# Performance work log

Hardware: AMD Instinct MI355X
Metric: run time of the kernel (lower is better)

## Reference

```python
import jax, jax.numpy as jnp
import numpy as np

B, N, E = 8, 20000, 320000
D_IN, D, D_OUT = 1, 64, 1
EPS = 1e-5


def _layer_norm(z, gamma, beta):
    mu = z.mean(-1, keepdims=True)
    var = ((z - mu) ** 2).mean(-1, keepdims=True)
    return gamma * (z - mu) / jnp.sqrt(var + EPS) + beta


def _mp_layer(h, src, dst, Ws, Wm, bias, gamma, beta):
    # h: (B, N, D); src/dst: (E,)
    h_self = h @ Ws                          # (B, N, D)
    msg = h[:, src, :] @ Wm                  # (B, E, D) gather + GEMM
    h_agg = jnp.zeros_like(h).at[:, dst, :].add(msg)   # scatter-add over nodes
    deg = jnp.zeros((N,), h.dtype).at[dst].add(1.0)
    deg = jnp.maximum(deg, 1.0)
    h_agg = h_agg / deg[None, :, None]
    z = h + jax.nn.relu(h_self + h_agg + bias)  # dropout = identity (eval)
    return _layer_norm(z, gamma, beta)


def setup_inputs() -> dict:
    key = jax.random.key(0)
    ks = jax.random.split(key, 16)
    # weights stored (in, out); y = x @ W + b. Kaiming-normal-ish scale.
    def kaiming(k, fin, fout):
        return jax.random.normal(k, (fin, fout), jnp.float32) * np.sqrt(2.0 / fin)
    inp = {
        "x": jax.random.normal(ks[0], (B, N, D_IN), jnp.float32),
        "edge_index": jax.random.randint(ks[1], (2, E), 0, N),
        "W_in": kaiming(ks[2], D_IN, D), "b_in": jnp.zeros((D,), jnp.float32),
        "Ws1": kaiming(ks[3], D, D), "Wm1": kaiming(ks[4], D, D),
        "bias1": jnp.zeros((D,), jnp.float32),
        "g1": jnp.ones((D,), jnp.float32), "be1": jnp.zeros((D,), jnp.float32),
        "Ws2": kaiming(ks[5], D, D), "Wm2": kaiming(ks[6], D, D),
        "bias2": jnp.zeros((D,), jnp.float32),
        "g2": jnp.ones((D,), jnp.float32), "be2": jnp.zeros((D,), jnp.float32),
        "Wh1": kaiming(ks[7], 2 * D, D), "bh1": jnp.zeros((D,), jnp.float32),
        "Wh2": kaiming(ks[8], D, D_OUT), "bh2": jnp.zeros((D_OUT,), jnp.float32),
    }
    return inp


def reference(x, edge_index, W_in, b_in, Ws1, Wm1, bias1, g1, be1,
              Ws2, Wm2, bias2, g2, be2, Wh1, bh1, Wh2, bh2):
    src, dst = edge_index[0], edge_index[1]
    h = jax.nn.relu(x @ W_in + b_in)                       # (B, N, D)
    h = _mp_layer(h, src, dst, Ws1, Wm1, bias1, g1, be1)
    h = _mp_layer(h, src, dst, Ws2, Wm2, bias2, g2, be2)
    graph_emb = jnp.concatenate([h.mean(axis=1), h.max(axis=1)], axis=-1)  # (B, 2D)
    out = jax.nn.relu(graph_emb @ Wh1 + bh1) @ Wh2 + bh2   # (B, D_OUT)
    return out
```

## Files before the change

### kernel.cpp

```cpp
#include <hip/hip_runtime.h>

#define BB 8
#define NN 20000
#define EE 320000
#define DD 64
#define ROWS (BB*NN)
#define TILES (ROWS/16)
#define EPS 1e-5f
#define CH 64


typedef __attribute__((ext_vector_type(4))) float float4v;
typedef __attribute__((ext_vector_type(8))) _Float16 half8v;
typedef __attribute__((ext_vector_type(4))) _Float16 half4v;

__device__ __forceinline__ int bcasti(int v, int l) {
  return __builtin_amdgcn_readlane(v, l);
}

__global__ __launch_bounds__(256) void k_encoder(const float* __restrict__ x,
    const float* __restrict__ Win, const float* __restrict__ bin,
    float* __restrict__ hN, _Float16* __restrict__ hH) {
  int idx = blockIdx.x * 256 + threadIdx.x;
  int g = idx * 4;
  if (g < NN * 512) {
    int n = g >> 9;
    int b = (g >> 6) & 7;
    int d0 = g & 63;
    float xv = x[(size_t)b * NN + n];
    float4 wv = *(const float4*)&Win[d0];
    float4 bv = *(const float4*)&bin[d0];
    float4 o;
    o.x = fmaf(xv, wv.x, bv.x); o.x = o.x > 0.f ? o.x : 0.f;
    o.y = fmaf(xv, wv.y, bv.y); o.y = o.y > 0.f ? o.y : 0.f;
    o.z = fmaf(xv, wv.z, bv.z); o.z = o.z > 0.f ? o.z : 0.f;
    o.w = fmaf(xv, wv.w, bv.w); o.w = o.w > 0.f ? o.w : 0.f;
    *(float4*)&hN[g] = o;
    half4v ho;
    ho[0] = (_Float16)o.x; ho[1] = (_Float16)o.y;
    ho[2] = (_Float16)o.z; ho[3] = (_Float16)o.w;
    *(half4v*)&hH[g] = ho;
  }
}

__global__ __launch_bounds__(256) void k_deg(const int* __restrict__ dst,
                                             int* __restrict__ cnt) {
  int e = blockIdx.x * 256 + threadIdx.x;
  if (e < EE) atomicAdd(&cnt[dst[e]], 1);
}

__global__ __launch_bounds__(1024) void k_scan(const int* __restrict__ cnt,
                                               int* __restrict__ rowptr) {
  __shared__ int part[1024];
  int t = threadIdx.x;
  const int PER = (NN + 1023) / 1024;
  int base = t * PER;
  int s = 0;
#pragma unroll
  for (int i = 0; i < PER; ++i) {
    int idx = base + i;
    s += (idx < NN) ? cnt[idx] : 0;
  }
  part[t] = s;
  __syncthreads();
  for (int off = 1; off < 1024; off <<= 1) {
    int v = (t >= off) ? part[t - off] : 0;
    __syncthreads();
    part[t] += v;
    __syncthreads();
  }
  int run = (t > 0) ? part[t - 1] : 0;
#pragma unroll
  for (int i = 0; i < PER; ++i) {
    int idx = base + i;
    if (idx <= NN) rowptr[idx] = run;
    run += (idx < NN) ? cnt[idx] : 0;
  }
}

__global__ __launch_bounds__(256) void k_fill(const int* __restrict__ src,
    const int* __restrict__ dst, const int* __restrict__ rowptr,
    int* __restrict__ cur, int* __restrict__ nbr) {
  int e = blockIdx.x * 256 + threadIdx.x;
  if (e < EE) {
    int t = dst[e];
    int pos = rowptr[t] + atomicAdd(&cur[t], 1);
    nbr[pos] = src[e];
  }
}

__global__ __launch_bounds__(256) void k_agg(const _Float16* __restrict__ hH,
    const int* __restrict__ rowptr, const int* __restrict__ nbr,
    _Float16* __restrict__ aggH) {
  int wid = (blockIdx.x * 256 + threadIdx.x) >> 6;
  int lane = threadIdx.x & 63;
  if (wid >= NN) return;
  int n = wid;
  int s0 = rowptr[n], s1 = rowptr[n + 1];
  float acc[8];
#pragma unroll
  for (int k = 0; k < 8; ++k) acc[k] = 0.f;
  for (int base = s0; base < s1; base += 64) {
    int m = s1 - base;
    if (m > 64) m = 64;
    int idxv = (base + lane < s1) ? nbr[base + lane] : 0;
    int j = 0;
    for (; j + 8 <= m; j += 8) {
      half8v v[8];
#pragma unroll
      for (int i = 0; i < 8; ++i) {
        int s = bcasti(idxv, j + i);
        v[i] = *(const half8v*)(hH + (size_t)s * 512 + lane * 8);
      }
#pragma unroll
      for (int k = 0; k < 8; ++k) {
        float t0 = (float)v[0][k] + (float)v[1][k];
        float t1 = (float)v[2][k] + (float)v[3][k];
        float t2 = (float)v[4][k] + (float)v[5][k];
        float t3 = (float)v[6][k] + (float)v[7][k];
        acc[k] += (t0 + t1) + (t2 + t3);
      }
    }
    for (; j + 4 <= m; j += 4) {
      half8v v[4];
#pragma unroll
      for (int i = 0; i < 4; ++i) {
        int s = bcasti(idxv, j + i);
        v[i] = *(const half8v*)(hH + (size_t)s * 512 + lane * 8);
      }
#pragma unroll
      for (int k = 0; k < 8; ++k) {
        acc[k] += ((float)v[0][k] + (float)v[1][k]) +
                  ((float)v[2][k] + (float)v[3][k]);
      }
    }
    for (; j < m; ++j) {
      int s = bcasti(idxv, j);
      half8v v = *(const half8v*)(hH + (size_t)s * 512 + lane * 8);
#pragma unroll
      for (int k = 0; k < 8; ++k) acc[k] += (float)v[k];
    }
  }
  int deg = s1 - s0;
  float iv = 1.0f / (float)(deg > 1 ? deg : 1);
  half8v o;
#pragma unroll
  for (int k = 0; k < 8; ++k) o[k] = (_Float16)(acc[k] * iv);
  *(half8v*)(aggH + (size_t)n * 512 + lane * 8) = o;
}

__global__ __launch_bounds__(256) void k_node_mfma(const float* __restrict__ hN,
    const _Float16* __restrict__ hH, const _Float16* __restrict__ aggH,
    const float* __restrict__ Ws, const float* __restrict__ Wm,
    const float* __restrict__ bias, const float* __restrict__ g,
    const float* __restrict__ be, float* __restrict__ outN,
    _Float16* __restrict__ outH, int nwaves_total) {
  __shared__ _Float16 ldsw[16384];
  int tid = threadIdx.x;
  int lane = tid & 63;
  int cidx = lane & 15;
  int grp = lane >> 4;

  for (int m = 0; m < 2; ++m) {
    const float* W = m ? Wm : Ws;
    for (int slot = tid; slot < 512; slot += 256) {
      int c = slot >> 8;
      int t = (slot >> 6) & 3;
      int l = slot & 63;
      int k0 = c * 32 + (l >> 4) * 8;
      int col = t * 16 + (l & 15);
      half8v ohi, olo;
#pragma unroll
      for (int i = 0; i < 8; ++i) {
        float w = W[(k0 + i) * DD + col];
        _Float16 hi = (_Float16)w;
        ohi[i] = hi;
        olo[i] = (_Float16)(w - (float)hi);
      }
      int ohf = (((m * 2 + 0) * 2 + c) * 4 + t) * 512 + l * 8;
      int olf = (((m * 2 + 1) * 2 + c) * 4 + t) * 512 + l * 8;
      *(half8v*)&ldsw[ohf] = ohi;
      *(half8v*)&ldsw[olf] = olo;
    }
  }
  __syncthreads();

  float bias_c[4], gam_c[4], bet_c[4];
#pragma unroll
  for (int t = 0; t < 4; ++t) {
    int c = t * 16 + cidx;
    bias_c[t] = bias[c];
    gam_c[t] = g[c];
    bet_c[t] = be[c];
  }

  int gwave = blockIdx.x * 4 + (tid >> 6);
  for (int tile = gwave; tile < TILES; tile += nwaves_total) {
    int r0 = tile * 16;
    const _Float16* hp = hH + (size_t)(r0 + cidx) * DD;
    const _Float16* ap = aggH + (size_t)(r0 + cidx) * DD;
    half8v ah[2], am[2];
    ah[0] = *(const half8v*)(hp + grp * 8);
    ah[1] = *(const half8v*)(hp + 32 + grp * 8);
    am[0] = *(const half8v*)(ap + grp * 8);
    am[1] = *(const half8v*)(ap + 32 + grp * 8);

    float4v acc[4];
#pragma unroll
    for (int t = 0; t < 4; ++t) acc[t] = (float4v){0.f, 0.f, 0.f, 0.f};
#pragma unroll
    for (int t = 0; t < 4; ++t) {
#pragma unroll
      for (int c = 0; c < 2; ++c) {
        const half8v bsh = *(const half8v*)&ldsw[((0 * 2 + c) * 4 + t) * 512 + lane * 8];
        const half8v bsl = *(const half8v*)&ldsw[((2 + c) * 4 + t) * 512 + lane * 8];
        const half8v bmh = *(const half8v*)&ldsw[((4 + c) * 4 + t) * 512 + lane * 8];
        const half8v bml = *(const half8v*)&ldsw[((6 + c) * 4 + t) * 512 + lane * 8];
        acc[t] = __builtin_amdgcn_mfma_f32_16x16x32_f16(ah[c], bsh, acc[t], 0, 0, 0);
        acc[t] = __builtin_amdgcn_mfma_f32_16x16x32_f16(ah[c], bsl, acc[t], 0, 0, 0);
        acc[t] = __builtin_amdgcn_mfma_f32_16x16x32_f16(am[c], bmh, acc[t], 0, 0, 0);
        acc[t] = __builtin_amdgcn_mfma_f32_16x16x32_f16(am[c], bml, acc[t], 0, 0, 0);
      }
    }
#pragma unroll
    for (int j = 0; j < 4; ++j) {
      int row = r0 + grp * 4 + j;
      const float* hr = hN + (size_t)row * DD;
      float zz[4];
      float part = 0.f;
#pragma unroll
      for (int t = 0; t < 4; ++t) {
        float hv = hr[t * 16 + cidx];
        float v = acc[t][j] + bias_c[t];
        v = v > 0.f ? v : 0.f;
        zz[t] = hv + v;
        part += zz[t];
      }
      part += __shfl_xor(part, 1);
      part += __shfl_xor(part, 2);
      part += __shfl_xor(part, 4);
      part += __shfl_xor(part, 8);
      float mu = part * (1.0f / 64.0f);
      float vs = 0.f;
#pragma unroll
      for (int t = 0; t < 4; ++t) {
        float d = zz[t] - mu;
        vs += d * d;
      }
      vs += __shfl_xor(vs, 1);
      vs += __shfl_xor(vs, 2);
      vs += __shfl_xor(vs, 4);
      vs += __shfl_xor(vs, 8);
      float inv = rsqrtf(vs * (1.0f / 64.0f) + EPS);
#pragma unroll
      for (int t = 0; t < 4; ++t) {
        float val = fmaf(gam_c[t] * (zz[t] - mu), inv, bet_c[t]);
        outN[(size_t)row * DD + t * 16 + cidx] = val;
        if (outH) outH[(size_t)row * DD + t * 16 + cidx] = (_Float16)val;
      }
    }
  }
}

__global__ __launch_bounds__(256) void k_reduce(const float* __restrict__ hN,
    float* __restrict__ psum, float* __restrict__ pmax) {
  int lane = threadIdx.x & 63;
  int w = threadIdx.x >> 6;
  int b = blockIdx.x / CH;
  int chunk = blockIdx.x % CH;
  const int csz = (NN + CH - 1) / CH;
  int n0 = chunk * csz;
  int n1 = n0 + csz;
  if (n1 > NN) n1 = NN;
  float s = 0.f, m = -INFINITY;
  for (int n = n0 + w; n < n1; n += 4) {
    float v = hN[(size_t)n * 512 + b * 64 + lane];
    s += v;
    m = fmaxf(m, v);
  }
  __shared__ float ls[4][DD], lm[4][DD];
  ls[w][lane] = s;
  lm[w][lane] = m;
  __syncthreads();
  if (w == 0) {
    float ss = ls[0][lane] + ls[1][lane] + ls[2][lane] + ls[3][lane];
    float mm = fmaxf(fmaxf(lm[0][lane], lm[1][lane]),
                     fmaxf(lm[2][lane], lm[3][lane]));
    psum[((size_t)b * CH + chunk) * DD + lane] = ss;
    pmax[((size_t)b * CH + chunk) * DD + lane] = mm;
  }
}

__global__ __launch_bounds__(512) void k_final(const float* __restrict__ psum,
    const float* __restrict__ pmax, const float* __restrict__ Wh1,
    const float* __restrict__ bh1, const float* __restrict__ Wh2,
    const float* __restrict__ bh2, float* __restrict__ out) {
  __shared__ float emb[BB][2 * DD];
  __shared__ float hid[BB][DD];
  int t = threadIdx.x;
  int b = t >> 6, d = t & 63;
  float s = 0.f, m = -INFINITY;
  for (int c = 0; c < CH; ++c) {
    s += psum[((size_t)b * CH + c) * DD + d];
    m = fmaxf(m, pmax[((size_t)b * CH + c) * DD + d]);
  }
  emb[b][d] = s * (1.0f / (float)NN);
  emb[b][DD + d] = m;
  __syncthreads();
  float acc = bh1[d];
#pragma unroll
  for (int k = 0; k < 2 * DD; ++k) acc = fmaf(emb[b][k], Wh1[k * DD + d], acc);
  hid[b][d] = acc > 0.f ? acc : 0.f;
  __syncthreads();
  if (d == 0) {
    float o = bh2[0];
    for (int j = 0; j < DD; ++j) o = fmaf(hid[b][j], Wh2[j], o);
    out[b] = o;
  }
}

extern "C" void kernel_launch(void* const* d_in, const int* in_sizes, int n_in,
                              void* d_out, int out_size, void* d_ws, size_t ws_size,
                              hipStream_t stream) {
  const float* x    = (const float*)d_in[0];
  const int*   ei   = (const int*)d_in[1];
  const float* Win  = (const float*)d_in[2];
  const float* bin  = (const float*)d_in[3];
  const float* Ws1  = (const float*)d_in[4];
  const float* Wm1  = (const float*)d_in[5];
  const float* bias1= (const float*)d_in[6];
  const float* g1   = (const float*)d_in[7];
  const float* be1  = (const float*)d_in[8];
  const float* Ws2  = (const float*)d_in[9];
  const float* Wm2  = (const float*)d_in[10];
  const float* bias2= (const float*)d_in[11];
  const float* g2   = (const float*)d_in[12];
  const float* be2  = (const float*)d_in[13];
  const float* Wh1  = (const float*)d_in[14];
  const float* bh1  = (const float*)d_in[15];
  const float* Wh2  = (const float*)d_in[16];
  const float* bh2  = (const float*)d_in[17];
  float* out = (float*)d_out;

  const int* src = ei;
  const int* dst = ei + EE;

  char* ws = (char*)d_ws;
  size_t off = 0;
  auto carve = [&](size_t bytes) {
    void* p = ws + off;
    off = (off + bytes + 255) & ~(size_t)255;
    return p;
  };
  const size_t hbytes = sizeof(float) * (size_t)ROWS * DD;
  float*    hA     = (float*)carve(hbytes);
  float*    hB     = (float*)carve(hbytes);
  _Float16* aggH   = (_Float16*)carve(hbytes / 2);
  _Float16* hH     = (_Float16*)carve(hbytes / 2);
  int*      cnt    = (int*)carve(sizeof(int) * NN);
  int*      rowptr = (int*)carve(sizeof(int) * (NN + 1));
  int*      nbr    = (int*)carve(sizeof(int) * EE);
  float*    psum   = (float*)carve(sizeof(float) * (size_t)BB * CH * DD);
  float*    pmax   = (float*)carve(sizeof(float) * (size_t)BB * CH * DD);

  const int NODE_BLOCKS = 2048;
  const int NODE_WAVES = NODE_BLOCKS * 4;

  k_encoder<<<(NN * 512 / 4 + 255) / 256, 256, 0, stream>>>(x, Win, bin, hA, hH);

  hipMemsetAsync(cnt, 0, sizeof(int) * NN, stream);
  k_deg<<<(EE + 255) / 256, 256, 0, stream>>>(dst, cnt);
  k_scan<<<1, 1024, 0, stream>>>(cnt, rowptr);
  hipMemsetAsync(cnt, 0, sizeof(int) * NN, stream);
  k_fill<<<(EE + 255) / 256, 256, 0, stream>>>(src, dst, rowptr, cnt, nbr);

  k_agg<<<(NN + 3) / 4, 256, 0, stream>>>(hH, rowptr, nbr, aggH);
  k_node_mfma<<<NODE_BLOCKS, 256, 0, stream>>>(hA, hH, aggH, Ws1, Wm1, bias1,
                                               g1, be1, hB, hH, NODE_WAVES);

  k_agg<<<(NN + 3) / 4, 256, 0, stream>>>(hH, rowptr, nbr, aggH);
  k_node_mfma<<<NODE_BLOCKS, 256, 0, stream>>>(hB, hH, aggH, Ws2, Wm2, bias2,
                                               g2, be2, hA, (_Float16*)nullptr,
                                               NODE_WAVES);

  k_reduce<<<BB * CH, 256, 0, stream>>>(hA, psum, pmax);
  k_final<<<1, 512, 0, stream>>>(psum, pmax, Wh1, bh1, Wh2, bh2, out);
}
```

Before: 263.9 us.

## Drop fp32 node-state buffers, keep hidden state in fp16 only, fold memsets

Removes the fp32 copy of the node features. The residual path, the layer-norm output and the final reduction now read and write fp16 buffers, which roughly halves the bytes moved by the node and reduce kernels. The count zeroing is folded into the encoder, and the scan writes each node's start offset straight into the fill cursor array, so both memset calls and the extra rowptr read in fill go away. The cost is lower precision: the residual and the pooled values now come from fp16-rounded activations.

```diff
diff --git a/kernel.cpp b/kernel.cpp
--- a/kernel.cpp
+++ b/kernel.cpp
@@ -12,7 +12,6 @@
 
 typedef __attribute__((ext_vector_type(4))) float float4v;
 typedef __attribute__((ext_vector_type(8))) _Float16 half8v;
-typedef __attribute__((ext_vector_type(4))) _Float16 half4v;
 
 __device__ __forceinline__ int bcasti(int v, int l) {
   return __builtin_amdgcn_readlane(v, l);
@@ -20,26 +19,28 @@
 
 __global__ __launch_bounds__(256) void k_encoder(const float* __restrict__ x,
     const float* __restrict__ Win, const float* __restrict__ bin,
-    float* __restrict__ hN, _Float16* __restrict__ hH) {
+    _Float16* __restrict__ hH, int* __restrict__ cnt) {
   int idx = blockIdx.x * 256 + threadIdx.x;
-  int g = idx * 4;
+  if (idx < NN) cnt[idx] = 0;
+  int g = idx * 8;
   if (g < NN * 512) {
     int n = g >> 9;
     int b = (g >> 6) & 7;
     int d0 = g & 63;
     float xv = x[(size_t)b * NN + n];
-    float4 wv = *(const float4*)&Win[d0];
-    float4 bv = *(const float4*)&bin[d0];
-    float4 o;
-    o.x = fmaf(xv, wv.x, bv.x); o.x = o.x > 0.f ? o.x : 0.f;
-    o.y = fmaf(xv, wv.y, bv.y); o.y = o.y > 0.f ? o.y : 0.f;
-    o.z = fmaf(xv, wv.z, bv.z); o.z = o.z > 0.f ? o.z : 0.f;
-    o.w = fmaf(xv, wv.w, bv.w); o.w = o.w > 0.f ? o.w : 0.f;
-    *(float4*)&hN[g] = o;
-    half4v ho;
-    ho[0] = (_Float16)o.x; ho[1] = (_Float16)o.y;
-    ho[2] = (_Float16)o.z; ho[3] = (_Float16)o.w;
-    *(half4v*)&hH[g] = ho;
+    float4 w0 = *(const float4*)&Win[d0];
+    float4 w1 = *(const float4*)&Win[d0 + 4];
+    float4 b0 = *(const float4*)&bin[d0];
+    float4 b1 = *(const float4*)&bin[d0 + 4];
+    float o[8];
+    o[0] = fmaf(xv, w0.x, b0.x); o[1] = fmaf(xv, w0.y, b0.y);
+    o[2] = fmaf(xv, w0.z, b0.z); o[3] = fmaf(xv, w0.w, b0.w);
+    o[4] = fmaf(xv, w1.x, b1.x); o[5] = fmaf(xv, w1.y, b1.y);
+    o[6] = fmaf(xv, w1.z, b1.z); o[7] = fmaf(xv, w1.w, b1.w);
+    half8v ho;
+#pragma unroll
+    for (int k = 0; k < 8; ++k) ho[k] = (_Float16)(o[k] > 0.f ? o[k] : 0.f);
+    *(half8v*)&hH[g] = ho;
   }
 }
 
@@ -50,7 +51,8 @@
 }
 
 __global__ __launch_bounds__(1024) void k_scan(const int* __restrict__ cnt,
-                                               int* __restrict__ rowptr) {
+                                               int* __restrict__ rowptr,
+                                               int* __restrict__ cur) {
   __shared__ int part[1024];
   int t = threadIdx.x;
   const int PER = (NN + 1023) / 1024;
@@ -74,17 +76,17 @@
   for (int i = 0; i < PER; ++i) {
     int idx = base + i;
     if (idx <= NN) rowptr[idx] = run;
+    if (idx < NN) cur[idx] = run;
     run += (idx < NN) ? cnt[idx] : 0;
   }
 }
 
 __global__ __launch_bounds__(256) void k_fill(const int* __restrict__ src,
-    const int* __restrict__ dst, const int* __restrict__ rowptr,
-    int* __restrict__ cur, int* __restrict__ nbr) {
+    const int* __restrict__ dst, int* __restrict__ cur,
+    int* __restrict__ nbr) {
   int e = blockIdx.x * 256 + threadIdx.x;
   if (e < EE) {
-    int t = dst[e];
-    int pos = rowptr[t] + atomicAdd(&cur[t], 1);
+    int pos = atomicAdd(&cur[dst[e]], 1);
     nbr[pos] = src[e];
   }
 }
@@ -149,12 +151,12 @@
   *(half8v*)(aggH + (size_t)n * 512 + lane * 8) = o;
 }
 
-__global__ __launch_bounds__(256) void k_node_mfma(const float* __restrict__ hN,
+__global__ __launch_bounds__(256) void k_node_mfma(
     const _Float16* __restrict__ hH, const _Float16* __restrict__ aggH,
     const float* __restrict__ Ws, const float* __restrict__ Wm,
     const float* __restrict__ bias, const float* __restrict__ g,
-    const float* __restrict__ be, float* __restrict__ outN,
-    _Float16* __restrict__ outH, int nwaves_total) {
+    const float* __restrict__ be, _Float16* __restrict__ outH,
+    int nwaves_total) {
   __shared__ _Float16 ldsw[16384];
   int tid = threadIdx.x;
   int lane = tid & 63;
@@ -177,10 +179,8 @@
         ohi[i] = hi;
         olo[i] = (_Float16)(w - (float)hi);
       }
-      int ohf = (((m * 2 + 0) * 2 + c) * 4 + t) * 512 + l * 8;
-      int olf = (((m * 2 + 1) * 2 + c) * 4 + t) * 512 + l * 8;
-      *(half8v*)&ldsw[ohf] = ohi;
-      *(half8v*)&ldsw[olf] = olo;
+      *(half8v*)&ldsw[(((m * 2 + 0) * 2 + c) * 4 + t) * 512 + l * 8] = ohi;
+      *(half8v*)&ldsw[(((m * 2 + 1) * 2 + c) * 4 + t) * 512 + l * 8] = olo;
     }
   }
   __syncthreads();
@@ -212,7 +212,7 @@
     for (int t = 0; t < 4; ++t) {
 #pragma unroll
       for (int c = 0; c < 2; ++c) {
-        const half8v bsh = *(const half8v*)&ldsw[((0 * 2 + c) * 4 + t) * 512 + lane * 8];
+        const half8v bsh = *(const half8v*)&ldsw[((0 + c) * 4 + t) * 512 + lane * 8];
         const half8v bsl = *(const half8v*)&ldsw[((2 + c) * 4 + t) * 512 + lane * 8];
         const half8v bmh = *(const half8v*)&ldsw[((4 + c) * 4 + t) * 512 + lane * 8];
         const half8v bml = *(const half8v*)&ldsw[((6 + c) * 4 + t) * 512 + lane * 8];
@@ -225,12 +225,12 @@
 #pragma unroll
     for (int j = 0; j < 4; ++j) {
       int row = r0 + grp * 4 + j;
-      const float* hr = hN + (size_t)row * DD;
+      const _Float16* hr = hH + (size_t)row * DD;
       float zz[4];
       float part = 0.f;
 #pragma unroll
       for (int t = 0; t < 4; ++t) {
-        float hv = hr[t * 16 + cidx];
+        float hv = (float)hr[t * 16 + cidx];
         float v = acc[t][j] + bias_c[t];
         v = v > 0.f ? v : 0.f;
         zz[t] = hv + v;
@@ -255,14 +255,13 @@
 #pragma unroll
       for (int t = 0; t < 4; ++t) {
         float val = fmaf(gam_c[t] * (zz[t] - mu), inv, bet_c[t]);
-        outN[(size_t)row * DD + t * 16 + cidx] = val;
-        if (outH) outH[(size_t)row * DD + t * 16 + cidx] = (_Float16)val;
-      }
-    }
-  }
-}
-
-__global__ __launch_bounds__(256) void k_reduce(const float* __restrict__ hN,
+        outH[(size_t)row * DD + t * 16 + cidx] = (_Float16)val;
+      }
+    }
+  }
+}
+
+__global__ __launch_bounds__(256) void k_reduce(const _Float16* __restrict__ hH,
     float* __restrict__ psum, float* __restrict__ pmax) {
   int lane = threadIdx.x & 63;
   int w = threadIdx.x >> 6;
@@ -274,7 +273,7 @@
   if (n1 > NN) n1 = NN;
   float s = 0.f, m = -INFINITY;
   for (int n = n0 + w; n < n1; n += 4) {
-    float v = hN[(size_t)n * 512 + b * 64 + lane];
+    float v = (float)hH[(size_t)n * 512 + b * 64 + lane];
     s += v;
     m = fmaxf(m, v);
   }
@@ -352,12 +351,12 @@
     off = (off + bytes + 255) & ~(size_t)255;
     return p;
   };
-  const size_t hbytes = sizeof(float) * (size_t)ROWS * DD;
-  float*    hA     = (float*)carve(hbytes);
-  float*    hB     = (float*)carve(hbytes);
-  _Float16* aggH   = (_Float16*)carve(hbytes / 2);
-  _Float16* hH     = (_Float16*)carve(hbytes / 2);
+  const size_t h16bytes = sizeof(_Float16) * (size_t)ROWS * DD;
+  _Float16* hA     = (_Float16*)carve(h16bytes);
+  _Float16* hB     = (_Float16*)carve(h16bytes);
+  _Float16* aggH   = (_Float16*)carve(h16bytes);
   int*      cnt    = (int*)carve(sizeof(int) * NN);
+  int*      cur    = (int*)carve(sizeof(int) * NN);
   int*      rowptr = (int*)carve(sizeof(int) * (NN + 1));
   int*      nbr    = (int*)carve(sizeof(int) * EE);
   float*    psum   = (float*)carve(sizeof(float) * (size_t)BB * CH * DD);
@@ -366,22 +365,19 @@
   const int NODE_BLOCKS = 2048;
   const int NODE_WAVES = NODE_BLOCKS * 4;
 
-  k_encoder<<<(NN * 512 / 4 + 255) / 256, 256, 0, stream>>>(x, Win, bin, hA, hH);
-
-  hipMemsetAsync(cnt, 0, sizeof(int) * NN, stream);
+  k_encoder<<<(NN * 512 / 8 + 255) / 256, 256, 0, stream>>>(x, Win, bin, hA, cnt);
+
   k_deg<<<(EE + 255) / 256, 256, 0, stream>>>(dst, cnt);
-  k_scan<<<1, 1024, 0, stream>>>(cnt, rowptr);
-  hipMemsetAsync(cnt, 0, sizeof(int) * NN, stream);
-  k_fill<<<(EE + 255) / 256, 256, 0, stream>>>(src, dst, rowptr, cnt, nbr);
-
-  k_agg<<<(NN + 3) / 4, 256, 0, stream>>>(hH, rowptr, nbr, aggH);
-  k_node_mfma<<<NODE_BLOCKS, 256, 0, stream>>>(hA, hH, aggH, Ws1, Wm1, bias1,
-                                               g1, be1, hB, hH, NODE_WAVES);
-
-  k_agg<<<(NN + 3) / 4, 256, 0, stream>>>(hH, rowptr, nbr, aggH);
-  k_node_mfma<<<NODE_BLOCKS, 256, 0, stream>>>(hB, hH, aggH, Ws2, Wm2, bias2,
-                                               g2, be2, hA, (_Float16*)nullptr,
-                                               NODE_WAVES);
+  k_scan<<<1, 1024, 0, stream>>>(cnt, rowptr, cur);
+  k_fill<<<(EE + 255) / 256, 256, 0, stream>>>(src, dst, cur, nbr);
+
+  k_agg<<<(NN + 3) / 4, 256, 0, stream>>>(hA, rowptr, nbr, aggH);
+  k_node_mfma<<<NODE_BLOCKS, 256, 0, stream>>>(hA, aggH, Ws1, Wm1, bias1, g1,
+                                               be1, hB, NODE_WAVES);
+
+  k_agg<<<(NN + 3) / 4, 256, 0, stream>>>(hB, rowptr, nbr, aggH);
+  k_node_mfma<<<NODE_BLOCKS, 256, 0, stream>>>(hB, aggH, Ws2, Wm2, bias2, g2,
+                                               be2, hA, NODE_WAVES);
 
   k_reduce<<<BB * CH, 256, 0, stream>>>(hA, psum, pmax);
   k_final<<<1, 512, 0, stream>>>(psum, pmax, Wh1, bh1, Wh2, bh2, out);
```

Result: faster. 248.3 us (-5.9%).
